# Kernel tuning notes

Measured on AMD Instinct MI355X. Metric: run time of the kernel, lower is better.

## Reference

```python
import jax, jax.numpy as jnp
import numpy as np

# MPI 15-joint skeleton: 0 head,1 neck,2 rsho,3 relb,4 rwri,5 lsho,6 lelb,7 lwri,
# 8 rhip,9 rknee,10 rankle,11 lhip,12 lknee,13 lankle,14 hip/spine
LEFT_BONES = np.array([[1, 5], [5, 6], [6, 7], [14, 11], [11, 12], [12, 13]], dtype=np.int32)
RIGHT_BONES = np.array([[1, 2], [2, 3], [3, 4], [14, 8], [8, 9], [9, 10]], dtype=np.int32)

FLEN = 512.0   # focal length (pixels)
CX, CY = 512.0, 256.0  # principal point
R_CAM = np.eye(3, dtype=np.float32)  # fixed drone->camera rotation

B, J = 262144, 15


def setup_inputs() -> dict:
    key = jax.random.key(0)
    k1, k2, k3, k4 = jax.random.split(key, 4)
    pose3d = jax.random.normal(k1, (B, 3, J), dtype=jnp.float32)
    pose_2d = jax.random.normal(k2, (B, 2, J), dtype=jnp.float32)
    # near-identity rotations so camera-frame depth stays well away from 0
    R_drone = jnp.eye(3, dtype=jnp.float32)[None] + 0.05 * jax.random.normal(k3, (B, 3, 3), dtype=jnp.float32)
    C_drone = jax.random.normal(k4, (B, 3, 1), dtype=jnp.float32)
    C_drone = C_drone.at[:, 2, :].add(-5.0)  # put camera behind the pose along z
    return {"pose3d": pose3d, "pose_2d": pose_2d, "R_drone": R_drone, "C_drone": C_drone}


def _forward(pose3d, pose_2d, R_drone, C_drone):
    lb = jnp.asarray(LEFT_BONES)
    rb = jnp.asarray(RIGHT_BONES)
    # bone length (squared) for each side: gather endpoints, diff, sum over xyz
    dl = pose3d[:, :, lb[:, 0]] - pose3d[:, :, lb[:, 1]]   # [B,3,6]
    dr = pose3d[:, :, rb[:, 0]] - pose3d[:, :, rb[:, 1]]   # [B,3,6]
    len_l = jnp.sum(dl * dl, axis=1)                        # [B,6]
    len_r = jnp.sum(dr * dr, axis=1)                        # [B,6]
    sym = jnp.mean((len_l - len_r) ** 2)                    # mean over bones and batch

    # take_bone_projection: camera frame = R_cam @ R_drone^T @ (P - C), pinhole projection
    P = jnp.einsum('bji,bjk->bik', R_drone, pose3d - C_drone)          # R_drone^T @ (P - C), [B,3,J]
    P = jnp.einsum('ij,bjk->bik', jnp.asarray(R_CAM), P)               # [B,3,J]
    z = P[:, 2]                                                         # [B,J]
    u = FLEN * P[:, 0] / z + CX
    v = FLEN * P[:, 1] / z + CY
    projected_2d = jnp.stack([u, v], axis=1)                            # [B,2,J]
    proj = jnp.mean((projected_2d - pose_2d) ** 2)
    return jnp.stack([sym, proj])


def reference(pose3d, pose_2d, R_drone, C_drone):
    return _forward(pose3d, pose_2d, R_drone, C_drone)
```

## Files before the change

kernel.cpp:

```cpp
#include <hip/hip_runtime.h>


typedef const __attribute__((address_space(1))) void* gas1_t;
typedef __attribute__((address_space(3))) void* las3_t;

__device__ __forceinline__ void gl16(const float* g, float* l) {
    __builtin_amdgcn_global_load_lds((gas1_t)g, (las3_t)l, 16, 0, 0);
}
__device__ __forceinline__ void gl4(const float* g, float* l) {
    __builtin_amdgcn_global_load_lds((gas1_t)g, (las3_t)l, 4, 0, 0);
}

#define SLABS 4

__global__ __launch_bounds__(64) void pose_calib_main(
    const float* __restrict__ pose3d,
    const float* __restrict__ pose2d,
    const float* __restrict__ Rd,
    const float* __restrict__ Cd,
    double* __restrict__ partial,
    int B)
{
    __shared__ float sX[2880];
    __shared__ float sP2[1920];
    __shared__ float sR[576];
    __shared__ float sC[192];

    const int lane = threadIdx.x;
    double sym_d = 0.0, proj_d = 0.0;

    const long long slab0 = (long long)blockIdx.x * SLABS;

    for (int s = 0; s < SLABS; ++s) {
        const long long p0 = (slab0 + s) * 64;
        if (p0 >= (long long)B) break;
        const bool full = (p0 + 64 <= (long long)B);

        float X[45], pu[15], pv[15], Rr[9], Cc[3];
        bool active;

        if (full) {
            if (s > 0)
                asm volatile("s_waitcnt lgkmcnt(0)" ::: "memory");

            const float* g3 = pose3d + p0 * 45;
            const float* g2 = pose2d + p0 * 30;
            const float* gR = Rd + p0 * 9;
            const float* gC = Cd + p0 * 3;

            #pragma unroll
            for (int k = 0; k < 11; ++k) gl16(g3 + k * 256 + lane * 4, sX + k * 256);
            gl4(g3 + 2816 + lane, sX + 2816);
            #pragma unroll
            for (int k = 0; k < 7; ++k) gl16(g2 + k * 256 + lane * 4, sP2 + k * 256);
            gl4(g2 + 1792 + lane, sP2 + 1792);
            gl4(g2 + 1856 + lane, sP2 + 1856);
            gl16(gR + lane * 4, sR);
            gl16(gR + 256 + lane * 4, sR + 256);
            gl4(gR + 512 + lane, sR + 512);
            gl4(gC + lane, sC);
            gl4(gC + 64 + lane, sC + 64);
            gl4(gC + 128 + lane, sC + 128);

            asm volatile("s_waitcnt vmcnt(0)" ::: "memory");

            active = true;
            #pragma unroll
            for (int i = 0; i < 45; ++i) X[i] = sX[lane * 45 + i];
            #pragma unroll
            for (int j = 0; j < 15; ++j) { pu[j] = sP2[lane * 30 + j]; pv[j] = sP2[lane * 30 + 15 + j]; }
            #pragma unroll
            for (int k = 0; k < 9; ++k) Rr[k] = sR[lane * 9 + k];
            #pragma unroll
            for (int c = 0; c < 3; ++c) Cc[c] = sC[lane * 3 + c];
        } else {
            const long long p = p0 + lane;
            active = (p < (long long)B);
            if (active) {
                const float* g3 = pose3d + p * 45;
                const float* g2 = pose2d + p * 30;
                const float* gR = Rd + p * 9;
                const float* gC = Cd + p * 3;
                #pragma unroll
                for (int i = 0; i < 45; ++i) X[i] = g3[i];
                #pragma unroll
                for (int j = 0; j < 15; ++j) { pu[j] = g2[j]; pv[j] = g2[15 + j]; }
                #pragma unroll
                for (int k = 0; k < 9; ++k) Rr[k] = gR[k];
                #pragma unroll
                for (int c = 0; c < 3; ++c) Cc[c] = gC[c];
            }
        }

        if (active) {
            const int lb0[6] = {1, 5, 6, 14, 11, 12}, lb1[6] = {5, 6, 7, 11, 12, 13};
            const int rb0[6] = {1, 2, 3, 14, 8, 9},   rb1[6] = {2, 3, 4, 8, 9, 10};
            #pragma unroll
            for (int k = 0; k < 6; ++k) {
                double ll = 0.0, lr = 0.0;
                #pragma unroll
                for (int c = 0; c < 3; ++c) {
                    double dl = (double)X[c * 15 + lb0[k]] - (double)X[c * 15 + lb1[k]];
                    double dr = (double)X[c * 15 + rb0[k]] - (double)X[c * 15 + rb1[k]];
                    ll += dl * dl;
                    lr += dr * dr;
                }
                double d = ll - lr;
                sym_d += d * d;
            }

            const double R00 = Rr[0], R01 = Rr[1], R02 = Rr[2];
            const double R10 = Rr[3], R11 = Rr[4], R12 = Rr[5];
            const double R20 = Rr[6], R21 = Rr[7], R22 = Rr[8];
            const double C0 = Cc[0], C1 = Cc[1], C2 = Cc[2];
            #pragma unroll
            for (int j = 0; j < 15; ++j) {
                double q0 = (double)X[j]      - C0;
                double q1 = (double)X[15 + j] - C1;
                double q2 = (double)X[30 + j] - C2;
                double P0 = R00 * q0 + R10 * q1 + R20 * q2;
                double P1 = R01 * q0 + R11 * q1 + R21 * q2;
                double P2 = R02 * q0 + R12 * q1 + R22 * q2;
                double rz = 1.0 / P2;
                double du = 512.0 * P0 * rz + 512.0 - (double)pu[j];
                double dv = 512.0 * P1 * rz + 256.0 - (double)pv[j];
                proj_d += du * du + dv * dv;
            }
        }
    }

    #pragma unroll
    for (int off = 32; off > 0; off >>= 1) {
        sym_d  += __shfl_down(sym_d,  off, 64);
        proj_d += __shfl_down(proj_d, off, 64);
    }
    if (lane == 0) {
        partial[2 * (size_t)blockIdx.x]     = sym_d;
        partial[2 * (size_t)blockIdx.x + 1] = proj_d;
    }
}

__global__ __launch_bounds__(256) void pose_calib_finish(
    const double* __restrict__ partial, int nblk,
    float* __restrict__ out, double inv_n_sym, double inv_n_proj)
{
    const double2* p2 = (const double2*)partial;
    double ss = 0.0, pp = 0.0;
    for (int i = threadIdx.x; i < nblk; i += 256) {
        double2 v = p2[i];
        ss += v.x;
        pp += v.y;
    }
    #pragma unroll
    for (int off = 32; off > 0; off >>= 1) {
        ss += __shfl_down(ss, off, 64);
        pp += __shfl_down(pp, off, 64);
    }
    __shared__ double s_s[4], s_p[4];
    const int lane = threadIdx.x & 63;
    const int wid  = threadIdx.x >> 6;
    if (lane == 0) { s_s[wid] = ss; s_p[wid] = pp; }
    __syncthreads();
    if (threadIdx.x == 0) {
        double S = s_s[0] + s_s[1] + s_s[2] + s_s[3];
        double P = s_p[0] + s_p[1] + s_p[2] + s_p[3];
        out[0] = (float)(S * inv_n_sym);
        out[1] = (float)(P * inv_n_proj);
    }
}

extern "C" void kernel_launch(void* const* d_in, const int* in_sizes, int n_in,
                              void* d_out, int out_size, void* d_ws, size_t ws_size,
                              hipStream_t stream) {
    const float* pose3d = (const float*)d_in[0];
    const float* pose2d = (const float*)d_in[1];
    const float* Rd     = (const float*)d_in[2];
    const float* Cd     = (const float*)d_in[3];

    const int B = in_sizes[3] / 3;
    const int nslab = (B + 63) / 64;
    const int nblk  = (nslab + SLABS - 1) / SLABS;

    double* partial = (double*)d_ws;

    pose_calib_main<<<nblk, 64, 0, stream>>>(pose3d, pose2d, Rd, Cd, partial, B);
    pose_calib_finish<<<1, 256, 0, stream>>>(
        partial, nblk, (float*)d_out,
        1.0 / ((double)B * 6.0), 1.0 / ((double)B * 30.0));
}
```

Baseline: 26.66 us.

## Double-buffer LDS staging in a persistent grid-stride loop

Replaces the fixed four-slab-per-block launch with a persistent grid of 1024 single-wave blocks that stride over 64-pose slabs. Each block double-buffers LDS, issuing the global-to-LDS loads for the next slab before computing the current one, with a partial vmcnt wait so memory and compute overlap. Tail loads are rewritten as overlapping 16-byte copies in place of 4-byte ones, and the partial-slab remainder moves to a single block after the loop. This adds hand-tuned waitcnt counts that must match the exact number of issued loads, and it cuts the grid from about 1024 blocks of four slabs to 1024 persistent blocks with fewer waves resident per CU.

Measured after the change: 30.58 us. 14.7% more time.

```diff
diff --git a/kernel.cpp b/kernel.cpp
--- a/kernel.cpp
+++ b/kernel.cpp
@@ -7,11 +7,47 @@
 __device__ __forceinline__ void gl16(const float* g, float* l) {
     __builtin_amdgcn_global_load_lds((gas1_t)g, (las3_t)l, 16, 0, 0);
 }
-__device__ __forceinline__ void gl4(const float* g, float* l) {
-    __builtin_amdgcn_global_load_lds((gas1_t)g, (las3_t)l, 4, 0, 0);
+
+#define NBLK 1024
+
+__device__ __forceinline__ void compute_pose_f64(
+    const float* __restrict__ X, const float* __restrict__ pu,
+    const float* __restrict__ pv, const float* __restrict__ Rr,
+    const float* __restrict__ Cc, double& sym_d, double& proj_d)
+{
+    const int lb0[6] = {1, 5, 6, 14, 11, 12}, lb1[6] = {5, 6, 7, 11, 12, 13};
+    const int rb0[6] = {1, 2, 3, 14, 8, 9},   rb1[6] = {2, 3, 4, 8, 9, 10};
+    #pragma unroll
+    for (int k = 0; k < 6; ++k) {
+        double ll = 0.0, lr = 0.0;
+        #pragma unroll
+        for (int c = 0; c < 3; ++c) {
+            double dl = (double)X[c * 15 + lb0[k]] - (double)X[c * 15 + lb1[k]];
+            double dr = (double)X[c * 15 + rb0[k]] - (double)X[c * 15 + rb1[k]];
+            ll += dl * dl;
+            lr += dr * dr;
+        }
+        double d = ll - lr;
+        sym_d += d * d;
+    }
+    const double R00 = Rr[0], R01 = Rr[1], R02 = Rr[2];
+    const double R10 = Rr[3], R11 = Rr[4], R12 = Rr[5];
+    const double R20 = Rr[6], R21 = Rr[7], R22 = Rr[8];
+    const double C0 = Cc[0], C1 = Cc[1], C2 = Cc[2];
+    #pragma unroll
+    for (int j = 0; j < 15; ++j) {
+        double q0 = (double)X[j]      - C0;
+        double q1 = (double)X[15 + j] - C1;
+        double q2 = (double)X[30 + j] - C2;
+        double P0 = R00 * q0 + R10 * q1 + R20 * q2;
+        double P1 = R01 * q0 + R11 * q1 + R21 * q2;
+        double P2 = R02 * q0 + R12 * q1 + R22 * q2;
+        double rz = 1.0 / P2;
+        double du = 512.0 * P0 * rz + 512.0 - (double)pu[j];
+        double dv = 512.0 * P1 * rz + 256.0 - (double)pv[j];
+        proj_d += du * du + dv * dv;
+    }
 }
-
-#define SLABS 4
 
 __global__ __launch_bounds__(64) void pose_calib_main(
     const float* __restrict__ pose3d,
@@ -21,111 +57,86 @@
     double* __restrict__ partial,
     int B)
 {
-    __shared__ float sX[2880];
-    __shared__ float sP2[1920];
-    __shared__ float sR[576];
-    __shared__ float sC[192];
+    __shared__ float lds[2][5568];
 
-    const int lane = threadIdx.x;
+    const int lane  = threadIdx.x;
+    const int nslab = B >> 6;
     double sym_d = 0.0, proj_d = 0.0;
 
-    const long long slab0 = (long long)blockIdx.x * SLABS;
+    auto stage = [&](int s, int b) {
+        const float* g3 = pose3d + (size_t)s * 2880;
+        const float* g2 = pose2d + (size_t)s * 1920;
+        const float* gR = Rd     + (size_t)s * 576;
+        const float* gC = Cd     + (size_t)s * 192;
+        float* sX = &lds[b][0];
+        float* sP = &lds[b][2880];
+        float* sR = &lds[b][4800];
+        float* sC = &lds[b][5376];
+        #pragma unroll
+        for (int k = 0; k < 11; ++k) gl16(g3 + k * 256 + lane * 4, sX + k * 256);
+        gl16(g3 + 2624 + lane * 4, sX + 2624);
+        #pragma unroll
+        for (int k = 0; k < 7; ++k) gl16(g2 + k * 256 + lane * 4, sP + k * 256);
+        gl16(g2 + 1664 + lane * 4, sP + 1664);
+        gl16(gR + lane * 4, sR);
+        gl16(gR + 256 + lane * 4, sR + 256);
+        gl16(gR + 320 + lane * 4, sR + 320);
+        if (lane < 48) gl16(gC + lane * 4, sC);
+    };
 
-    for (int s = 0; s < SLABS; ++s) {
-        const long long p0 = (slab0 + s) * 64;
-        if (p0 >= (long long)B) break;
-        const bool full = (p0 + 64 <= (long long)B);
+    int  slab = blockIdx.x;
+    int  cur  = 0;
+    bool have = (slab < nslab);
+    if (have) stage(slab, 0);
 
-        float X[45], pu[15], pv[15], Rr[9], Cc[3];
-        bool active;
+    while (have) {
+        const int  nxt      = slab + NBLK;
+        const bool have_nxt = (nxt < nslab);
 
-        if (full) {
-            if (s > 0)
-                asm volatile("s_waitcnt lgkmcnt(0)" ::: "memory");
+        asm volatile("s_waitcnt lgkmcnt(0)" ::: "memory");
+        if (have_nxt) stage(nxt, cur ^ 1);
 
-            const float* g3 = pose3d + p0 * 45;
-            const float* g2 = pose2d + p0 * 30;
-            const float* gR = Rd + p0 * 9;
-            const float* gC = Cd + p0 * 3;
+        if (have_nxt) asm volatile("s_waitcnt vmcnt(24)" ::: "memory");
+        else          asm volatile("s_waitcnt vmcnt(0)"  ::: "memory");
+        __builtin_amdgcn_sched_barrier(0);
 
-            #pragma unroll
-            for (int k = 0; k < 11; ++k) gl16(g3 + k * 256 + lane * 4, sX + k * 256);
-            gl4(g3 + 2816 + lane, sX + 2816);
-            #pragma unroll
-            for (int k = 0; k < 7; ++k) gl16(g2 + k * 256 + lane * 4, sP2 + k * 256);
-            gl4(g2 + 1792 + lane, sP2 + 1792);
-            gl4(g2 + 1856 + lane, sP2 + 1856);
-            gl16(gR + lane * 4, sR);
-            gl16(gR + 256 + lane * 4, sR + 256);
-            gl4(gR + 512 + lane, sR + 512);
-            gl4(gC + lane, sC);
-            gl4(gC + 64 + lane, sC + 64);
-            gl4(gC + 128 + lane, sC + 128);
-
-            asm volatile("s_waitcnt vmcnt(0)" ::: "memory");
-
-            active = true;
+        {
+            const float* sX = &lds[cur][0];
+            const float* sP = &lds[cur][2880];
+            const float* sR = &lds[cur][4800];
+            const float* sC = &lds[cur][5376];
+            float X[45], pu[15], pv[15], Rr[9], Cc[3];
             #pragma unroll
             for (int i = 0; i < 45; ++i) X[i] = sX[lane * 45 + i];
             #pragma unroll
-            for (int j = 0; j < 15; ++j) { pu[j] = sP2[lane * 30 + j]; pv[j] = sP2[lane * 30 + 15 + j]; }
+            for (int j = 0; j < 15; ++j) { pu[j] = sP[lane * 30 + j]; pv[j] = sP[lane * 30 + 15 + j]; }
             #pragma unroll
             for (int k = 0; k < 9; ++k) Rr[k] = sR[lane * 9 + k];
             #pragma unroll
             for (int c = 0; c < 3; ++c) Cc[c] = sC[lane * 3 + c];
-        } else {
-            const long long p = p0 + lane;
-            active = (p < (long long)B);
-            if (active) {
-                const float* g3 = pose3d + p * 45;
-                const float* g2 = pose2d + p * 30;
-                const float* gR = Rd + p * 9;
-                const float* gC = Cd + p * 3;
-                #pragma unroll
-                for (int i = 0; i < 45; ++i) X[i] = g3[i];
-                #pragma unroll
-                for (int j = 0; j < 15; ++j) { pu[j] = g2[j]; pv[j] = g2[15 + j]; }
-                #pragma unroll
-                for (int k = 0; k < 9; ++k) Rr[k] = gR[k];
-                #pragma unroll
-                for (int c = 0; c < 3; ++c) Cc[c] = gC[c];
-            }
+            compute_pose_f64(X, pu, pv, Rr, Cc, sym_d, proj_d);
         }
 
-        if (active) {
-            const int lb0[6] = {1, 5, 6, 14, 11, 12}, lb1[6] = {5, 6, 7, 11, 12, 13};
-            const int rb0[6] = {1, 2, 3, 14, 8, 9},   rb1[6] = {2, 3, 4, 8, 9, 10};
+        slab = nxt; have = have_nxt; cur ^= 1;
+    }
+
+    if ((B & 63) && blockIdx.x == (unsigned)(nslab % NBLK)) {
+        const int p = nslab * 64 + lane;
+        if (p < B) {
+            const float* g3 = pose3d + (size_t)p * 45;
+            const float* g2 = pose2d + (size_t)p * 30;
+            const float* gR = Rd + (size_t)p * 9;
+            const float* gC = Cd + (size_t)p * 3;
+            float X[45], pu[15], pv[15], Rr[9], Cc[3];
             #pragma unroll
-            for (int k = 0; k < 6; ++k) {
-                double ll = 0.0, lr = 0.0;
-                #pragma unroll
-                for (int c = 0; c < 3; ++c) {
-                    double dl = (double)X[c * 15 + lb0[k]] - (double)X[c * 15 + lb1[k]];
-                    double dr = (double)X[c * 15 + rb0[k]] - (double)X[c * 15 + rb1[k]];
-                    ll += dl * dl;
-                    lr += dr * dr;
-                }
-                double d = ll - lr;
-                sym_d += d * d;
-            }
-
-            const double R00 = Rr[0], R01 = Rr[1], R02 = Rr[2];
-            const double R10 = Rr[3], R11 = Rr[4], R12 = Rr[5];
-            const double R20 = Rr[6], R21 = Rr[7], R22 = Rr[8];
-            const double C0 = Cc[0], C1 = Cc[1], C2 = Cc[2];
+            for (int i = 0; i < 45; ++i) X[i] = g3[i];
             #pragma unroll
-            for (int j = 0; j < 15; ++j) {
-                double q0 = (double)X[j]      - C0;
-                double q1 = (double)X[15 + j] - C1;
-                double q2 = (double)X[30 + j] - C2;
-                double P0 = R00 * q0 + R10 * q1 + R20 * q2;
-                double P1 = R01 * q0 + R11 * q1 + R21 * q2;
-                double P2 = R02 * q0 + R12 * q1 + R22 * q2;
-                double rz = 1.0 / P2;
-                double du = 512.0 * P0 * rz + 512.0 - (double)pu[j];
-                double dv = 512.0 * P1 * rz + 256.0 - (double)pv[j];
-                proj_d += du * du + dv * dv;
-            }
+            for (int j = 0; j < 15; ++j) { pu[j] = g2[j]; pv[j] = g2[15 + j]; }
+            #pragma unroll
+            for (int k = 0; k < 9; ++k) Rr[k] = gR[k];
+            #pragma unroll
+            for (int c = 0; c < 3; ++c) Cc[c] = gC[c];
+            compute_pose_f64(X, pu, pv, Rr, Cc, sym_d, proj_d);
         }
     }
 
@@ -178,13 +189,11 @@
     const float* Cd     = (const float*)d_in[3];
 
     const int B = in_sizes[3] / 3;
-    const int nslab = (B + 63) / 64;
-    const int nblk  = (nslab + SLABS - 1) / SLABS;
 
     double* partial = (double*)d_ws;
 
-    pose_calib_main<<<nblk, 64, 0, stream>>>(pose3d, pose2d, Rd, Cd, partial, B);
+    pose_calib_main<<<NBLK, 64, 0, stream>>>(pose3d, pose2d, Rd, Cd, partial, B);
     pose_calib_finish<<<1, 256, 0, stream>>>(
-        partial, nblk, (float*)d_out,
+        partial, NBLK, (float*)d_out,
         1.0 / ((double)B * 6.0), 1.0 / ((double)B * 30.0));
 }
```
